# Kernel optimization log

Hardware: AMD Instinct MI355X
Metric: run time of the kernel (lower is better)

The kernel has to match this reference:

```python
import jax, jax.numpy as jnp
import numpy as np

N = 50000
E = 800000
D = 128
LN_EPS = 1e-5


def setup_inputs() -> dict:
    key = jax.random.key(0)
    k1, k2, k3, k4 = jax.random.split(key, 4)
    x = jax.random.normal(k1, (N, D), dtype=jnp.float32)
    edge_index = jax.random.randint(k2, (2, E), 0, N, dtype=jnp.int32)
    # xavier_uniform with gain=sqrt(2) (relu gain)
    gain = float(np.sqrt(2.0))
    lim_lin = gain * float(np.sqrt(6.0 / (D + D)))
    W_lin = jax.random.uniform(k3, (D, D), dtype=jnp.float32, minval=-lim_lin, maxval=lim_lin)
    lim_attn = gain * float(np.sqrt(6.0 / (2 * D + 1)))
    W_attn = jax.random.uniform(k4, (1, 2 * D), dtype=jnp.float32, minval=-lim_attn, maxval=lim_attn)
    ln_scale = jnp.ones((D,), dtype=jnp.float32)
    ln_bias = jnp.zeros((D,), dtype=jnp.float32)
    return {"x": x, "W_lin": W_lin, "W_attn": W_attn,
            "ln_scale": ln_scale, "ln_bias": ln_bias, "edge_index": edge_index}


def _layer_norm(h, scale, bias):
    mu = jnp.mean(h, axis=-1, keepdims=True)
    var = jnp.mean(jnp.square(h - mu), axis=-1, keepdims=True)
    return (h - mu) * jax.lax.rsqrt(var + LN_EPS) * scale + bias


def reference(x, W_lin, W_attn, ln_scale, ln_bias, edge_index):
    n = x.shape[0]
    src, dst = edge_index[0], edge_index[1]
    # h = x @ W_lin^T  [N, D]
    h = jnp.einsum('nd,od->no', x, W_lin)
    # attention score: [h_src || h_dst] @ W_attn^T == h_src@a_src + h_dst@a_dst
    d = h.shape[1]
    a_src = W_attn[0, :d]
    a_dst = W_attn[0, d:]
    s_src = h @ a_src  # [N]
    s_dst = h @ a_dst  # [N]
    scores = s_src[src] + s_dst[dst]  # [E]
    scores = jnp.where(scores >= 0, scores, 0.2 * scores)  # leaky_relu(0.2)
    # segment softmax over edges grouped by dst
    seg_max = jax.ops.segment_max(scores, dst, num_segments=n)  # [N]
    seg_max = jnp.where(jnp.isfinite(seg_max), seg_max, 0.0)
    ex = jnp.exp(scores - seg_max[dst])  # [E]
    denom = jax.ops.segment_sum(ex, dst, num_segments=n)  # [N]
    alpha = ex / jnp.where(denom > 0, denom, 1.0)[dst]  # [E]
    # weighted message aggregation (dropout is identity in eval mode)
    msgs = h[src] * alpha[:, None]  # [E, D]
    agg = jax.ops.segment_sum(msgs, dst, num_segments=n)  # [N, D]
    # residual (input_dim == output_dim -> no projection) + layer norm
    return _layer_norm(agg + x, ln_scale, ln_bias)
```

## Files before the change

### kernel.cpp

```cpp
#include <hip/hip_runtime.h>

#define N_NODES 50000
#define E_EDGES 800000
#define D_DIM   128
#define LN_EPS  1e-5f
#define SCAN_BLOCKS 196
#define GEMM_BLOCKS 391
#define HIST4_BLOCKS 782
#define SCAT_BLOCKS  782

typedef __bf16 bf16x8 __attribute__((ext_vector_type(8)));
typedef unsigned short ushort8v __attribute__((ext_vector_type(8)));
typedef float f32x4 __attribute__((ext_vector_type(4)));
typedef int i32x2v __attribute__((ext_vector_type(2)));
typedef int i32x16v __attribute__((ext_vector_type(16)));

__device__ inline unsigned short f2b(float f) {
    unsigned int u = __float_as_uint(f);
    unsigned int r = u + 0x7FFFu + ((u >> 16) & 1u);
    return (unsigned short)(r >> 16);
}
__device__ inline float b2f(unsigned short h) {
    return __uint_as_float((unsigned int)h << 16);
}
__device__ inline float blo(unsigned int u) { return __uint_as_float(u << 16); }
__device__ inline float bhi(unsigned int u) { return __uint_as_float(u & 0xFFFF0000u); }

__device__ inline i32x16v sload16(const uint2* p) {
    i32x16v r;
    asm volatile("s_load_dwordx16 %0, %1, 0x0\n\ts_waitcnt lgkmcnt(0)"
                 : "=&s"(r) : "s"(p));
    return r;
}
__device__ inline i32x2v sload2(const uint2* p) {
    i32x2v r;
    asm volatile("s_load_dwordx2 %0, %1, 0x0\n\ts_waitcnt lgkmcnt(0)"
                 : "=&s"(r) : "s"(p));
    return r;
}

__global__ void k_prep(const float* __restrict__ W,
                       unsigned short* __restrict__ Whp,
                       unsigned short* __restrict__ Wlp,
                       int* __restrict__ count) {
    int i = blockIdx.x * 256 + threadIdx.x;
    if (i < N_NODES) count[i] = 0;
    if (i < 16384) {
        int o = i >> 7, k = i & 127;
        float v = W[i];
        unsigned short h = f2b(v);
        unsigned short l = f2b(v - b2f(h));
        int idx = (k >> 3) * 1024 + o * 8 + (k & 7);
        Whp[idx] = h;
        Wlp[idx] = l;
    }
}

__global__ __launch_bounds__(256, 2) void k_gemm_hist(
        const float* __restrict__ x, const unsigned short* __restrict__ Wpk,
        const float* __restrict__ Wa, const int* __restrict__ dst,
        int* __restrict__ count, int* __restrict__ erank,
        unsigned short* __restrict__ hb,
        float* __restrict__ ssrc, float* __restrict__ sdst) {
    __shared__ float4 wl4[4096];
    const int tid = threadIdx.x;

    if (blockIdx.x >= GEMM_BLOCKS) {
        int e0 = (blockIdx.x - GEMM_BLOCKS) * 1024 + tid * 4;
        if (e0 < E_EDGES) {
            int4 dv = *(const int4*)&dst[e0];
            int r0 = atomicAdd(&count[dv.x], 1);
            int r1 = atomicAdd(&count[dv.y], 1);
            int r2 = atomicAdd(&count[dv.z], 1);
            int r3 = atomicAdd(&count[dv.w], 1);
            *(int4*)&erank[e0] = make_int4(r0, r1, r2, r3);
        }
        return;
    }

    {
        const float4* wsrc = (const float4*)Wpk;
        #pragma unroll
        for (int i = 0; i < 16; ++i)
            wl4[i * 256 + tid] = wsrc[i * 256 + tid];
    }

    const int c = tid & 15;
    const int g = (tid >> 4) & 3;
    const int w = tid >> 6;
    const int n0 = blockIdx.x * 128;

    bf16x8 ah[2][4], al[2][4];
    #pragma unroll
    for (int t = 0; t < 2; ++t) {
        int n = n0 + w * 32 + t * 16 + c;
        if (n > N_NODES - 1) n = N_NODES - 1;
        const float* xr = x + (size_t)n * 128;
        #pragma unroll
        for (int s = 0; s < 4; ++s) {
            float4 f0 = *(const float4*)(xr + s * 32 + g * 8);
            float4 f1 = *(const float4*)(xr + s * 32 + g * 8 + 4);
            float fv[8] = {f0.x, f0.y, f0.z, f0.w, f1.x, f1.y, f1.z, f1.w};
            ushort8v uh, ul;
            #pragma unroll
            for (int j = 0; j < 8; ++j) {
                unsigned short hj = f2b(fv[j]);
                uh[j] = hj;
                ul[j] = f2b(fv[j] - b2f(hj));
            }
            ah[t][s] = __builtin_bit_cast(bf16x8, uh);
            al[t][s] = __builtin_bit_cast(bf16x8, ul);
        }
    }

    __syncthreads();
    const bf16x8* wb = (const bf16x8*)wl4;

    f32x4 acc[2][8];
    #pragma unroll
    for (int t = 0; t < 2; ++t)
        #pragma unroll
        for (int cb = 0; cb < 8; ++cb)
            acc[t][cb] = (f32x4){0.f, 0.f, 0.f, 0.f};

    #pragma unroll
    for (int cb = 0; cb < 8; ++cb) {
        #pragma unroll
        for (int s = 0; s < 4; ++s) {
            int q = (s * 4 + g) * 128 + cb * 16 + c;
            bf16x8 bh = wb[q];
            bf16x8 bl = wb[2048 + q];
            acc[0][cb] = __builtin_amdgcn_mfma_f32_16x16x32_bf16(ah[0][s], bh, acc[0][cb], 0, 0, 0);
            acc[1][cb] = __builtin_amdgcn_mfma_f32_16x16x32_bf16(ah[1][s], bh, acc[1][cb], 0, 0, 0);
            acc[0][cb] = __builtin_amdgcn_mfma_f32_16x16x32_bf16(al[0][s], bh, acc[0][cb], 0, 0, 0);
            acc[1][cb] = __builtin_amdgcn_mfma_f32_16x16x32_bf16(al[1][s], bh, acc[1][cb], 0, 0, 0);
            acc[0][cb] = __builtin_amdgcn_mfma_f32_16x16x32_bf16(ah[0][s], bl, acc[0][cb], 0, 0, 0);
            acc[1][cb] = __builtin_amdgcn_mfma_f32_16x16x32_bf16(ah[1][s], bl, acc[1][cb], 0, 0, 0);
        }
    }

    float asv[8], adv[8];
    #pragma unroll
    for (int cb = 0; cb < 8; ++cb) {
        asv[cb] = Wa[cb * 16 + c];
        adv[cb] = Wa[128 + cb * 16 + c];
    }
    #pragma unroll
    for (int t = 0; t < 2; ++t) {
        #pragma unroll
        for (int i = 0; i < 4; ++i) {
            int n = n0 + w * 32 + t * 16 + g * 4 + i;
            float ps = 0.f, pd = 0.f;
            #pragma unroll
            for (int cb = 0; cb < 8; ++cb) {
                float v = acc[t][cb][i];
                ps += v * asv[cb];
                pd += v * adv[cb];
            }
            #pragma unroll
            for (int off = 1; off < 16; off <<= 1) {
                ps += __shfl_xor(ps, off);
                pd += __shfl_xor(pd, off);
            }
            if (c == 0 && n < N_NODES) { ssrc[n] = ps; sdst[n] = pd; }
        }
    }

    __syncthreads();
    unsigned short* hlds = (unsigned short*)wl4;
    #pragma unroll
    for (int t = 0; t < 2; ++t)
        #pragma unroll
        for (int cb = 0; cb < 8; ++cb)
            #pragma unroll
            for (int i = 0; i < 4; ++i)
                hlds[(w * 32 + t * 16 + g * 4 + i) * 128 + cb * 16 + c] =
                    f2b(acc[t][cb][i]);
    __syncthreads();
    #pragma unroll
    for (int ii = 0; ii < 8; ++ii) {
        int cidx = ii * 256 + tid;
        int row = cidx >> 4, off = cidx & 15;
        int n = n0 + row;
        if (n < N_NODES) {
            ushort8v v = *(const ushort8v*)&hlds[row * 128 + off * 8];
            *(ushort8v*)&hb[(size_t)n * 128 + off * 8] = v;
        }
    }
}

__global__ __launch_bounds__(256) void k_scan1(const int* __restrict__ count,
                                               int* __restrict__ rowptr,
                                               int* __restrict__ bsum) {
    __shared__ int wsum[4];
    const int tid  = threadIdx.x;
    const int lane = tid & 63, w = tid >> 6;
    int i = blockIdx.x * 256 + tid;
    int v = (i < N_NODES) ? count[i] : 0;
    int sc = v;
    #pragma unroll
    for (int off = 1; off < 64; off <<= 1) {
        int t = __shfl_up(sc, off);
        if (lane >= off) sc += t;
    }
    if (lane == 63) wsum[w] = sc;
    __syncthreads();
    if (tid == 0) {
        int s0 = wsum[0], s1 = wsum[1], s2 = wsum[2], s3 = wsum[3];
        wsum[0] = 0; wsum[1] = s0; wsum[2] = s0 + s1; wsum[3] = s0 + s1 + s2;
        bsum[blockIdx.x] = s0 + s1 + s2 + s3;
    }
    __syncthreads();
    if (i < N_NODES) rowptr[i] = sc - v + wsum[w];
}

__global__ __launch_bounds__(256) void k_scan2(int* __restrict__ bsum) {
    __shared__ int wsum[4];
    const int tid  = threadIdx.x;
    const int lane = tid & 63, w = tid >> 6;
    int v = (tid < SCAN_BLOCKS) ? bsum[tid] : 0;
    int sc = v;
    #pragma unroll
    for (int off = 1; off < 64; off <<= 1) {
        int t = __shfl_up(sc, off);
        if (lane >= off) sc += t;
    }
    if (lane == 63) wsum[w] = sc;
    __syncthreads();
    if (tid == 0) {
        int s0 = wsum[0], s1 = wsum[1], s2 = wsum[2];
        wsum[3] = s0 + s1 + s2; wsum[2] = s0 + s1; wsum[1] = s0; wsum[0] = 0;
    }
    __syncthreads();
    if (tid < SCAN_BLOCKS) bsum[tid] = sc - v + wsum[w];
}

__global__ __launch_bounds__(256) void k_scatter(
        const int* __restrict__ src, const int* __restrict__ dst,
        const int* __restrict__ erank,
        const float* __restrict__ ssrc, const float* __restrict__ sdst,
        const int* __restrict__ rowptr, const int* __restrict__ bsum,
        uint2* __restrict__ sev) {
    int e0 = (blockIdx.x * 256 + threadIdx.x) * 4;
    if (e0 >= E_EDGES) return;
    int4 sv = *(const int4*)&src[e0];
    int4 dv = *(const int4*)&dst[e0];
    int4 rk = *(const int4*)&erank[e0];
    float ss0 = ssrc[sv.x], ss1 = ssrc[sv.y], ss2 = ssrc[sv.z], ss3 = ssrc[sv.w];
    float sd0 = sdst[dv.x], sd1 = sdst[dv.y], sd2 = sdst[dv.z], sd3 = sdst[dv.w];
    int rp0 = rowptr[dv.x], rp1 = rowptr[dv.y], rp2 = rowptr[dv.z], rp3 = rowptr[dv.w];
    int bs0 = bsum[dv.x >> 8], bs1 = bsum[dv.y >> 8];
    int bs2 = bsum[dv.z >> 8], bs3 = bsum[dv.w >> 8];
    float c0 = ss0 + sd0, c1 = ss1 + sd1, c2 = ss2 + sd2, c3 = ss3 + sd3;
    c0 = c0 >= 0.f ? c0 : 0.2f * c0;
    c1 = c1 >= 0.f ? c1 : 0.2f * c1;
    c2 = c2 >= 0.f ? c2 : 0.2f * c2;
    c3 = c3 >= 0.f ? c3 : 0.2f * c3;
    sev[rp0 + bs0 + rk.x] = make_uint2((unsigned int)sv.x, __float_as_uint(__expf(c0)));
    sev[rp1 + bs1 + rk.y] = make_uint2((unsigned int)sv.y, __float_as_uint(__expf(c1)));
    sev[rp2 + bs2 + rk.z] = make_uint2((unsigned int)sv.z, __float_as_uint(__expf(c2)));
    sev[rp3 + bs3 + rk.w] = make_uint2((unsigned int)sv.w, __float_as_uint(__expf(c3)));
}

__global__ __launch_bounds__(256) void k_gather(
        const int* __restrict__ rowptr, const int* __restrict__ bsum,
        const uint2* __restrict__ sev,
        const unsigned short* __restrict__ hb, const float* __restrict__ x,
        const float* __restrict__ scale, const float* __restrict__ bias,
        float* __restrict__ out) {
    int n    = __builtin_amdgcn_readfirstlane(blockIdx.x * 4 + (threadIdx.x >> 6));
    int lane = threadIdx.x & 63;
    int beg = rowptr[n] + bsum[n >> 8];
    int end = (n == N_NODES - 1) ? E_EDGES : rowptr[n + 1] + bsum[(n + 1) >> 8];
    const unsigned int* hb32 = (const unsigned int*)hb;

    float a0 = 0.f, a1 = 0.f, b0 = 0.f, b1 = 0.f, den = 0.f, den2 = 0.f;

    int i = beg;
    for (; i + 15 < end; i += 16) {
        int ib = __builtin_amdgcn_readfirstlane(i);
        i32x16v s0 = sload16(sev + ib);
        i32x16v s1 = sload16(sev + ib + 8);
        unsigned int u[16];
        #pragma unroll
        for (int q = 0; q < 8; ++q)
            u[q] = hb32[(((unsigned)s0[2 * q]) << 6) + lane];
        #pragma unroll
        for (int q = 0; q < 8; ++q)
            u[8 + q] = hb32[(((unsigned)s1[2 * q]) << 6) + lane];
        #pragma unroll
        for (int q = 0; q < 8; q += 2) {
            float ex0 = __uint_as_float(s0[2 * q + 1]);
            float ex1 = __uint_as_float(s0[2 * q + 3]);
            den  += ex0; den2 += ex1;
            a0 += ex0 * blo(u[q]);     a1 += ex0 * bhi(u[q]);
            b0 += ex1 * blo(u[q + 1]); b1 += ex1 * bhi(u[q + 1]);
        }
        #pragma unroll
        for (int q = 0; q < 8; q += 2) {
            float ex0 = __uint_as_float(s1[2 * q + 1]);
            float ex1 = __uint_as_float(s1[2 * q + 3]);
            den  += ex0; den2 += ex1;
            a0 += ex0 * blo(u[8 + q]);     a1 += ex0 * bhi(u[8 + q]);
            b0 += ex1 * blo(u[8 + q + 1]); b1 += ex1 * bhi(u[8 + q + 1]);
        }
    }
    for (; i + 7 < end; i += 8) {
        int ib = __builtin_amdgcn_readfirstlane(i);
        i32x16v s0 = sload16(sev + ib);
        unsigned int u[8];
        #pragma unroll
        for (int q = 0; q < 8; ++q)
            u[q] = hb32[(((unsigned)s0[2 * q]) << 6) + lane];
        #pragma unroll
        for (int q = 0; q < 8; q += 2) {
            float ex0 = __uint_as_float(s0[2 * q + 1]);
            float ex1 = __uint_as_float(s0[2 * q + 3]);
            den  += ex0; den2 += ex1;
            a0 += ex0 * blo(u[q]);     a1 += ex0 * bhi(u[q]);
            b0 += ex1 * blo(u[q + 1]); b1 += ex1 * bhi(u[q + 1]);
        }
    }
    for (; i < end; ++i) {
        i32x2v p2 = sload2(sev + __builtin_amdgcn_readfirstlane(i));
        unsigned int u0 = hb32[(((unsigned)p2[0]) << 6) + lane];
        float ex0 = __uint_as_float(p2[1]);
        den += ex0;
        a0 += ex0 * blo(u0);
        a1 += ex0 * bhi(u0);
    }
    a0 += b0; a1 += b1; den += den2;

    float inv_d = 1.f / (den > 0.f ? den : 1.f);
    size_t base = (size_t)n * 128 + 2 * lane;
    float2 xv = *(const float2*)&x[base];
    float r0 = a0 * inv_d + xv.x;
    float r1 = a1 * inv_d + xv.y;

    float sum = r0 + r1;
    #pragma unroll
    for (int off = 32; off >= 1; off >>= 1) sum += __shfl_xor(sum, off);
    float mu = sum * (1.f / 128.f);
    float d0 = r0 - mu, d1 = r1 - mu;
    float ss = d0 * d0 + d1 * d1;
    #pragma unroll
    for (int off = 32; off >= 1; off >>= 1) ss += __shfl_xor(ss, off);
    float inv = rsqrtf(ss * (1.f / 128.f) + LN_EPS);
    float o0 = d0 * inv * scale[2 * lane]     + bias[2 * lane];
    float o1 = d1 * inv * scale[2 * lane + 1] + bias[2 * lane + 1];
    *(float2*)&out[base] = make_float2(o0, o1);
}

extern "C" void kernel_launch(void* const* d_in, const int* in_sizes, int n_in,
                              void* d_out, int out_size, void* d_ws, size_t ws_size,
                              hipStream_t stream) {
    const float* x        = (const float*)d_in[0];
    const float* W_lin    = (const float*)d_in[1];
    const float* W_attn   = (const float*)d_in[2];
    const float* ln_scale = (const float*)d_in[3];
    const float* ln_bias  = (const float*)d_in[4];
    const int*   edge     = (const int*)d_in[5];
    const int*   e_src    = edge;
    const int*   e_dst    = edge + E_EDGES;
    float* out = (float*)d_out;

    char* ws = (char*)d_ws;
    unsigned short* hb  = (unsigned short*)(ws);
    unsigned short* Whp = (unsigned short*)(ws + 12800000);
    unsigned short* Wlp = (unsigned short*)(ws + 12832768);
    float* ssrc   = (float*)(ws + 12865536);
    float* sdst   = (float*)(ws + 13065536);
    int*   count  = (int*)  (ws + 13265536);
    int*   rowptr = (int*)  (ws + 13465536);
    int*   bsum   = (int*)  (ws + 13665552);
    uint2* sev    = (uint2*)(ws + 13666352);
    int*   erank  = (int*)  (ws + 20066352);

    k_prep     <<<SCAN_BLOCKS, 256, 0, stream>>>(W_lin, Whp, Wlp, count);
    k_gemm_hist<<<GEMM_BLOCKS + HIST4_BLOCKS, 256, 0, stream>>>(
                    x, Whp, W_attn, e_dst, count, erank, hb, ssrc, sdst);
    k_scan1    <<<SCAN_BLOCKS, 256, 0, stream>>>(count, rowptr, bsum);
    k_scan2    <<<1,    256, 0, stream>>>(bsum);
    k_scatter  <<<SCAT_BLOCKS, 256, 0, stream>>>(e_src, e_dst, erank, ssrc, sdst,
                                                 rowptr, bsum, sev);
    k_gather   <<<12500, 256, 0, stream>>>(rowptr, bsum, sev, hb, x,
                                           ln_scale, ln_bias, out);
}
```

Before: 179.5 us.

## Split gather into column-sliced partial aggregation plus separate layernorm pass

Replaces the single per-node gather kernel with a column-sliced gather: each node's 128 features are split into four 32-column slices handled by separate waves, with two edges processed per wave using half-waves. Partial aggregates and denominators are written to global memory, and a new final kernel applies normalization, the residual and layernorm. The two scan kernels are merged using a last-block-done atomic, and scatter now handles 8 edges per thread. The aim is more parallelism and lower latency in the gather, at the cost of an extra full-size intermediate buffer round trip, 2-byte scattered loads instead of 4-byte ones, and an extra kernel launch.

Measured after the change: 258.5 us. +44.0%, slower.

```diff
diff --git a/kernel.cpp b/kernel.cpp
--- a/kernel.cpp
+++ b/kernel.cpp
@@ -7,7 +7,9 @@
 #define SCAN_BLOCKS 196
 #define GEMM_BLOCKS 391
 #define HIST4_BLOCKS 782
-#define SCAT_BLOCKS  782
+#define SCAT_BLOCKS  391
+#define GSLICE_BLOCKS 50000
+#define FINAL_BLOCKS 12500
 
 typedef __bf16 bf16x8 __attribute__((ext_vector_type(8)));
 typedef unsigned short ushort8v __attribute__((ext_vector_type(8)));
@@ -23,8 +25,6 @@
 __device__ inline float b2f(unsigned short h) {
     return __uint_as_float((unsigned int)h << 16);
 }
-__device__ inline float blo(unsigned int u) { return __uint_as_float(u << 16); }
-__device__ inline float bhi(unsigned int u) { return __uint_as_float(u & 0xFFFF0000u); }
 
 __device__ inline i32x16v sload16(const uint2* p) {
     i32x16v r;
@@ -42,8 +42,9 @@
 __global__ void k_prep(const float* __restrict__ W,
                        unsigned short* __restrict__ Whp,
                        unsigned short* __restrict__ Wlp,
-                       int* __restrict__ count) {
+                       int* __restrict__ count, int* __restrict__ done) {
     int i = blockIdx.x * 256 + threadIdx.x;
+    if (i == 0) *done = 0;
     if (i < N_NODES) count[i] = 0;
     if (i < 16384) {
         int o = i >> 7, k = i & 127;
@@ -57,7 +58,7 @@
 }
 
 __global__ __launch_bounds__(256, 2) void k_gemm_hist(
-        const float* __restrict__ x, const unsigned short* __restrict__ Wpk,
+        const float* __restrict__ xin, const unsigned short* __restrict__ Wpk,
         const float* __restrict__ Wa, const int* __restrict__ dst,
         int* __restrict__ count, int* __restrict__ erank,
         unsigned short* __restrict__ hb,
@@ -95,7 +96,7 @@
     for (int t = 0; t < 2; ++t) {
         int n = n0 + w * 32 + t * 16 + c;
         if (n > N_NODES - 1) n = N_NODES - 1;
-        const float* xr = x + (size_t)n * 128;
+        const float* xr = xin + (size_t)n * 128;
         #pragma unroll
         for (int s = 0; s < 4; ++s) {
             float4 f0 = *(const float4*)(xr + s * 32 + g * 8);
@@ -189,10 +190,12 @@
     }
 }
 
-__global__ __launch_bounds__(256) void k_scan1(const int* __restrict__ count,
-                                               int* __restrict__ rowptr,
-                                               int* __restrict__ bsum) {
+__global__ __launch_bounds__(256) void k_scan(const int* __restrict__ count,
+                                              int* __restrict__ rowptr,
+                                              int* __restrict__ bsum,
+                                              int* __restrict__ done) {
     __shared__ int wsum[4];
+    __shared__ int amLast;
     const int tid  = threadIdx.x;
     const int lane = tid & 63, w = tid >> 6;
     int i = blockIdx.x * 256 + tid;
@@ -212,27 +215,28 @@
     }
     __syncthreads();
     if (i < N_NODES) rowptr[i] = sc - v + wsum[w];
-}
-
-__global__ __launch_bounds__(256) void k_scan2(int* __restrict__ bsum) {
-    __shared__ int wsum[4];
-    const int tid  = threadIdx.x;
-    const int lane = tid & 63, w = tid >> 6;
-    int v = (tid < SCAN_BLOCKS) ? bsum[tid] : 0;
-    int sc = v;
+
+    __threadfence();
+    if (tid == 0) amLast = (atomicAdd(done, 1) == SCAN_BLOCKS - 1);
+    __syncthreads();
+    if (!amLast) return;
+    __threadfence();
+    int v2 = (tid < SCAN_BLOCKS) ? bsum[tid] : 0;
+    int sc2 = v2;
     #pragma unroll
     for (int off = 1; off < 64; off <<= 1) {
-        int t = __shfl_up(sc, off);
-        if (lane >= off) sc += t;
-    }
-    if (lane == 63) wsum[w] = sc;
+        int t = __shfl_up(sc2, off);
+        if (lane >= off) sc2 += t;
+    }
+    __syncthreads();
+    if (lane == 63) wsum[w] = sc2;
     __syncthreads();
     if (tid == 0) {
         int s0 = wsum[0], s1 = wsum[1], s2 = wsum[2];
         wsum[3] = s0 + s1 + s2; wsum[2] = s0 + s1; wsum[1] = s0; wsum[0] = 0;
     }
     __syncthreads();
-    if (tid < SCAN_BLOCKS) bsum[tid] = sc - v + wsum[w];
+    if (tid < SCAN_BLOCKS) bsum[tid] = sc2 - v2 + wsum[w];
 }
 
 __global__ __launch_bounds__(256) void k_scatter(
@@ -241,101 +245,90 @@
         const float* __restrict__ ssrc, const float* __restrict__ sdst,
         const int* __restrict__ rowptr, const int* __restrict__ bsum,
         uint2* __restrict__ sev) {
-    int e0 = (blockIdx.x * 256 + threadIdx.x) * 4;
+    int e0 = (blockIdx.x * 256 + threadIdx.x) * 8;
     if (e0 >= E_EDGES) return;
-    int4 sv = *(const int4*)&src[e0];
-    int4 dv = *(const int4*)&dst[e0];
-    int4 rk = *(const int4*)&erank[e0];
-    float ss0 = ssrc[sv.x], ss1 = ssrc[sv.y], ss2 = ssrc[sv.z], ss3 = ssrc[sv.w];
-    float sd0 = sdst[dv.x], sd1 = sdst[dv.y], sd2 = sdst[dv.z], sd3 = sdst[dv.w];
-    int rp0 = rowptr[dv.x], rp1 = rowptr[dv.y], rp2 = rowptr[dv.z], rp3 = rowptr[dv.w];
-    int bs0 = bsum[dv.x >> 8], bs1 = bsum[dv.y >> 8];
-    int bs2 = bsum[dv.z >> 8], bs3 = bsum[dv.w >> 8];
-    float c0 = ss0 + sd0, c1 = ss1 + sd1, c2 = ss2 + sd2, c3 = ss3 + sd3;
-    c0 = c0 >= 0.f ? c0 : 0.2f * c0;
-    c1 = c1 >= 0.f ? c1 : 0.2f * c1;
-    c2 = c2 >= 0.f ? c2 : 0.2f * c2;
-    c3 = c3 >= 0.f ? c3 : 0.2f * c3;
-    sev[rp0 + bs0 + rk.x] = make_uint2((unsigned int)sv.x, __float_as_uint(__expf(c0)));
-    sev[rp1 + bs1 + rk.y] = make_uint2((unsigned int)sv.y, __float_as_uint(__expf(c1)));
-    sev[rp2 + bs2 + rk.z] = make_uint2((unsigned int)sv.z, __float_as_uint(__expf(c2)));
-    sev[rp3 + bs3 + rk.w] = make_uint2((unsigned int)sv.w, __float_as_uint(__expf(c3)));
-}
-
-__global__ __launch_bounds__(256) void k_gather(
+    int sv[8], dv[8], rk[8];
+    *(int4*)&sv[0] = *(const int4*)&src[e0];
+    *(int4*)&sv[4] = *(const int4*)&src[e0 + 4];
+    *(int4*)&dv[0] = *(const int4*)&dst[e0];
+    *(int4*)&dv[4] = *(const int4*)&dst[e0 + 4];
+    *(int4*)&rk[0] = *(const int4*)&erank[e0];
+    *(int4*)&rk[4] = *(const int4*)&erank[e0 + 4];
+    float ssv[8], sdv[8];
+    int rp[8], bs[8];
+    #pragma unroll
+    for (int q = 0; q < 8; ++q) {
+        ssv[q] = ssrc[sv[q]];
+        sdv[q] = sdst[dv[q]];
+        rp[q]  = rowptr[dv[q]];
+        bs[q]  = bsum[dv[q] >> 8];
+    }
+    #pragma unroll
+    for (int q = 0; q < 8; ++q) {
+        float sc = ssv[q] + sdv[q];
+        sc = sc >= 0.f ? sc : 0.2f * sc;
+        sev[rp[q] + bs[q] + rk[q]] =
+            make_uint2((unsigned int)sv[q], __float_as_uint(__expf(sc)));
+    }
+}
+
+__global__ __launch_bounds__(256) void k_gslice(
         const int* __restrict__ rowptr, const int* __restrict__ bsum,
-        const uint2* __restrict__ sev,
-        const unsigned short* __restrict__ hb, const float* __restrict__ x,
+        const uint2* __restrict__ sev, const unsigned short* __restrict__ hb,
+        float* __restrict__ part, float* __restrict__ den) {
+    const int bid   = blockIdx.x;
+    const int xb    = bid & 7;
+    const int slice = xb >> 1;
+    const int grp   = (bid >> 3) * 2 + (xb & 1);
+    const int n     = __builtin_amdgcn_readfirstlane(grp * 4 + (threadIdx.x >> 6));
+    const int lane  = threadIdx.x & 63;
+    const int el    = lane >> 5, sl = lane & 31;
+    int beg = rowptr[n] + bsum[n >> 8];
+    int end = (n == N_NODES - 1) ? E_EDGES : rowptr[n + 1] + bsum[(n + 1) >> 8];
+    const unsigned short* hs = hb + slice * 32 + sl;
+
+    float a = 0.f, dn = 0.f;
+    int i = beg;
+    for (; i + 7 < end; i += 8) {
+        i32x16v s0 = sload16(sev + __builtin_amdgcn_readfirstlane(i));
+        #pragma unroll
+        for (int q = 0; q < 4; ++q) {
+            int srcA = s0[4 * q], srcB = s0[4 * q + 2];
+            float exA = __uint_as_float(s0[4 * q + 1]);
+            float exB = __uint_as_float(s0[4 * q + 3]);
+            int srcq = el ? srcB : srcA;
+            unsigned short u = hs[(size_t)srcq * 128];
+            float ex = el ? exB : exA;
+            a  += ex * b2f(u);
+            dn += exA + exB;
+        }
+    }
+    for (; i < end; ++i) {
+        i32x2v p2 = sload2(sev + __builtin_amdgcn_readfirstlane(i));
+        unsigned short u = hs[(size_t)p2[0] * 128];
+        float ex = __uint_as_float(p2[1]);
+        a  += (el ? 0.f : ex * b2f(u));
+        dn += ex;
+    }
+    a += __shfl_xor(a, 32);
+    if (lane < 32) part[(size_t)n * 128 + slice * 32 + sl] = a;
+    if (slice == 0 && lane == 0) den[n] = dn;
+}
+
+__global__ __launch_bounds__(256) void k_final(
+        const float* __restrict__ part, const float* __restrict__ den,
+        const float* __restrict__ xin,
         const float* __restrict__ scale, const float* __restrict__ bias,
         float* __restrict__ out) {
-    int n    = __builtin_amdgcn_readfirstlane(blockIdx.x * 4 + (threadIdx.x >> 6));
+    int n    = blockIdx.x * 4 + (threadIdx.x >> 6);
     int lane = threadIdx.x & 63;
-    int beg = rowptr[n] + bsum[n >> 8];
-    int end = (n == N_NODES - 1) ? E_EDGES : rowptr[n + 1] + bsum[(n + 1) >> 8];
-    const unsigned int* hb32 = (const unsigned int*)hb;
-
-    float a0 = 0.f, a1 = 0.f, b0 = 0.f, b1 = 0.f, den = 0.f, den2 = 0.f;
-
-    int i = beg;
-    for (; i + 15 < end; i += 16) {
-        int ib = __builtin_amdgcn_readfirstlane(i);
-        i32x16v s0 = sload16(sev + ib);
-        i32x16v s1 = sload16(sev + ib + 8);
-        unsigned int u[16];
-        #pragma unroll
-        for (int q = 0; q < 8; ++q)
-            u[q] = hb32[(((unsigned)s0[2 * q]) << 6) + lane];
-        #pragma unroll
-        for (int q = 0; q < 8; ++q)
-            u[8 + q] = hb32[(((unsigned)s1[2 * q]) << 6) + lane];
-        #pragma unroll
-        for (int q = 0; q < 8; q += 2) {
-            float ex0 = __uint_as_float(s0[2 * q + 1]);
-            float ex1 = __uint_as_float(s0[2 * q + 3]);
-            den  += ex0; den2 += ex1;
-            a0 += ex0 * blo(u[q]);     a1 += ex0 * bhi(u[q]);
-            b0 += ex1 * blo(u[q + 1]); b1 += ex1 * bhi(u[q + 1]);
-        }
-        #pragma unroll
-        for (int q = 0; q < 8; q += 2) {
-            float ex0 = __uint_as_float(s1[2 * q + 1]);
-            float ex1 = __uint_as_float(s1[2 * q + 3]);
-            den  += ex0; den2 += ex1;
-            a0 += ex0 * blo(u[8 + q]);     a1 += ex0 * bhi(u[8 + q]);
-            b0 += ex1 * blo(u[8 + q + 1]); b1 += ex1 * bhi(u[8 + q + 1]);
-        }
-    }
-    for (; i + 7 < end; i += 8) {
-        int ib = __builtin_amdgcn_readfirstlane(i);
-        i32x16v s0 = sload16(sev + ib);
-        unsigned int u[8];
-        #pragma unroll
-        for (int q = 0; q < 8; ++q)
-            u[q] = hb32[(((unsigned)s0[2 * q]) << 6) + lane];
-        #pragma unroll
-        for (int q = 0; q < 8; q += 2) {
-            float ex0 = __uint_as_float(s0[2 * q + 1]);
-            float ex1 = __uint_as_float(s0[2 * q + 3]);
-            den  += ex0; den2 += ex1;
-            a0 += ex0 * blo(u[q]);     a1 += ex0 * bhi(u[q]);
-            b0 += ex1 * blo(u[q + 1]); b1 += ex1 * bhi(u[q + 1]);
-        }
-    }
-    for (; i < end; ++i) {
-        i32x2v p2 = sload2(sev + __builtin_amdgcn_readfirstlane(i));
-        unsigned int u0 = hb32[(((unsigned)p2[0]) << 6) + lane];
-        float ex0 = __uint_as_float(p2[1]);
-        den += ex0;
-        a0 += ex0 * blo(u0);
-        a1 += ex0 * bhi(u0);
-    }
-    a0 += b0; a1 += b1; den += den2;
-
-    float inv_d = 1.f / (den > 0.f ? den : 1.f);
+    float dn = den[n];
+    float inv_d = 1.f / (dn > 0.f ? dn : 1.f);
     size_t base = (size_t)n * 128 + 2 * lane;
-    float2 xv = *(const float2*)&x[base];
-    float r0 = a0 * inv_d + xv.x;
-    float r1 = a1 * inv_d + xv.y;
+    float2 pv = *(const float2*)&part[base];
+    float2 xv = *(const float2*)&xin[base];
+    float r0 = pv.x * inv_d + xv.x;
+    float r1 = pv.y * inv_d + xv.y;
 
     float sum = r0 + r1;
     #pragma unroll
@@ -375,14 +368,17 @@
     int*   bsum   = (int*)  (ws + 13665552);
     uint2* sev    = (uint2*)(ws + 13666352);
     int*   erank  = (int*)  (ws + 20066352);
-
-    k_prep     <<<SCAN_BLOCKS, 256, 0, stream>>>(W_lin, Whp, Wlp, count);
+    float* part   = (float*)(ws + 23266432);
+    float* den    = (float*)(ws + 48866432);
+    int*   done   = (int*)  (ws + 49066432);
+
+    k_prep     <<<SCAN_BLOCKS, 256, 0, stream>>>(W_lin, Whp, Wlp, count, done);
     k_gemm_hist<<<GEMM_BLOCKS + HIST4_BLOCKS, 256, 0, stream>>>(
                     x, Whp, W_attn, e_dst, count, erank, hb, ssrc, sdst);
-    k_scan1    <<<SCAN_BLOCKS, 256, 0, stream>>>(count, rowptr, bsum);
-    k_scan2    <<<1,    256, 0, stream>>>(bsum);
+    k_scan     <<<SCAN_BLOCKS, 256, 0, stream>>>(count, rowptr, bsum, done);
     k_scatter  <<<SCAT_BLOCKS, 256, 0, stream>>>(e_src, e_dst, erank, ssrc, sdst,
                                                  rowptr, bsum, sev);
-    k_gather   <<<12500, 256, 0, stream>>>(rowptr, bsum, sev, hb, x,
-                                           ln_scale, ln_bias, out);
-}
+    k_gslice   <<<GSLICE_BLOCKS, 256, 0, stream>>>(rowptr, bsum, sev, hb, part, den);
+    k_final    <<<FINAL_BLOCKS, 256, 0, stream>>>(part, den, x,
+                                                  ln_scale, ln_bias, out);
+}
```

## Fuse scan passes via last-block pattern, halve scatter work per thread, overlap scalar loads

Applied to the files above, without the earlier changes.

The two-kernel prefix scan becomes one kernel: the last block to finish, detected through an atomic counter that k_prep resets, scans the block sums. This removes one kernel launch and its dependency gap. k_scatter now handles 2 edges per thread instead of 4, with twice as many blocks, to raise parallelism for the random gathers. In the gather kernel, the two scalar loads of each 16-edge chunk are issued back to back before a single wait, so their latencies overlap.

After: 189.9 us. 5.8% more time.

```diff
diff --git a/kernel.cpp b/kernel.cpp
--- a/kernel.cpp
+++ b/kernel.cpp
@@ -7,7 +7,8 @@
 #define SCAN_BLOCKS 196
 #define GEMM_BLOCKS 391
 #define HIST4_BLOCKS 782
-#define SCAT_BLOCKS  782
+#define SCAT_BLOCKS 1563
+#define GATH_BLOCKS 12500
 
 typedef __bf16 bf16x8 __attribute__((ext_vector_type(8)));
 typedef unsigned short ushort8v __attribute__((ext_vector_type(8)));
@@ -26,11 +27,14 @@
 __device__ inline float blo(unsigned int u) { return __uint_as_float(u << 16); }
 __device__ inline float bhi(unsigned int u) { return __uint_as_float(u & 0xFFFF0000u); }
 
-__device__ inline i32x16v sload16(const uint2* p) {
+__device__ inline i32x16v sload16_nw(const uint2* p) {
     i32x16v r;
-    asm volatile("s_load_dwordx16 %0, %1, 0x0\n\ts_waitcnt lgkmcnt(0)"
-                 : "=&s"(r) : "s"(p));
+    asm volatile("s_load_dwordx16 %0, %1, 0x0" : "=&s"(r) : "s"(p));
     return r;
+}
+__device__ inline void swait() {
+    asm volatile("s_waitcnt lgkmcnt(0)");
+    __builtin_amdgcn_sched_barrier(0);
 }
 __device__ inline i32x2v sload2(const uint2* p) {
     i32x2v r;
@@ -42,8 +46,9 @@
 __global__ void k_prep(const float* __restrict__ W,
                        unsigned short* __restrict__ Whp,
                        unsigned short* __restrict__ Wlp,
-                       int* __restrict__ count) {
+                       int* __restrict__ count, int* __restrict__ done) {
     int i = blockIdx.x * 256 + threadIdx.x;
+    if (i == 0) *done = 0;
     if (i < N_NODES) count[i] = 0;
     if (i < 16384) {
         int o = i >> 7, k = i & 127;
@@ -57,7 +62,7 @@
 }
 
 __global__ __launch_bounds__(256, 2) void k_gemm_hist(
-        const float* __restrict__ x, const unsigned short* __restrict__ Wpk,
+        const float* __restrict__ xin, const unsigned short* __restrict__ Wpk,
         const float* __restrict__ Wa, const int* __restrict__ dst,
         int* __restrict__ count, int* __restrict__ erank,
         unsigned short* __restrict__ hb,
@@ -95,7 +100,7 @@
     for (int t = 0; t < 2; ++t) {
         int n = n0 + w * 32 + t * 16 + c;
         if (n > N_NODES - 1) n = N_NODES - 1;
-        const float* xr = x + (size_t)n * 128;
+        const float* xr = xin + (size_t)n * 128;
         #pragma unroll
         for (int s = 0; s < 4; ++s) {
             float4 f0 = *(const float4*)(xr + s * 32 + g * 8);
@@ -189,10 +194,12 @@
     }
 }
 
-__global__ __launch_bounds__(256) void k_scan1(const int* __restrict__ count,
-                                               int* __restrict__ rowptr,
-                                               int* __restrict__ bsum) {
+__global__ __launch_bounds__(256) void k_scan(const int* __restrict__ count,
+                                              int* __restrict__ rowptr,
+                                              int* __restrict__ bsum,
+                                              int* __restrict__ done) {
     __shared__ int wsum[4];
+    __shared__ int amLast;
     const int tid  = threadIdx.x;
     const int lane = tid & 63, w = tid >> 6;
     int i = blockIdx.x * 256 + tid;
@@ -212,27 +219,28 @@
     }
     __syncthreads();
     if (i < N_NODES) rowptr[i] = sc - v + wsum[w];
-}
-
-__global__ __launch_bounds__(256) void k_scan2(int* __restrict__ bsum) {
-    __shared__ int wsum[4];
-    const int tid  = threadIdx.x;
-    const int lane = tid & 63, w = tid >> 6;
-    int v = (tid < SCAN_BLOCKS) ? bsum[tid] : 0;
-    int sc = v;
+
+    __threadfence();
+    if (tid == 0) amLast = (atomicAdd(done, 1) == SCAN_BLOCKS - 1);
+    __syncthreads();
+    if (!amLast) return;
+    __threadfence();
+    int v2 = (tid < SCAN_BLOCKS) ? bsum[tid] : 0;
+    int sc2 = v2;
     #pragma unroll
     for (int off = 1; off < 64; off <<= 1) {
-        int t = __shfl_up(sc, off);
-        if (lane >= off) sc += t;
-    }
-    if (lane == 63) wsum[w] = sc;
+        int t = __shfl_up(sc2, off);
+        if (lane >= off) sc2 += t;
+    }
+    __syncthreads();
+    if (lane == 63) wsum[w] = sc2;
     __syncthreads();
     if (tid == 0) {
         int s0 = wsum[0], s1 = wsum[1], s2 = wsum[2];
         wsum[3] = s0 + s1 + s2; wsum[2] = s0 + s1; wsum[1] = s0; wsum[0] = 0;
     }
     __syncthreads();
-    if (tid < SCAN_BLOCKS) bsum[tid] = sc - v + wsum[w];
+    if (tid < SCAN_BLOCKS) bsum[tid] = sc2 - v2 + wsum[w];
 }
 
 __global__ __launch_bounds__(256) void k_scatter(
@@ -241,25 +249,20 @@
         const float* __restrict__ ssrc, const float* __restrict__ sdst,
         const int* __restrict__ rowptr, const int* __restrict__ bsum,
         uint2* __restrict__ sev) {
-    int e0 = (blockIdx.x * 256 + threadIdx.x) * 4;
+    int e0 = (blockIdx.x * 256 + threadIdx.x) * 2;
     if (e0 >= E_EDGES) return;
-    int4 sv = *(const int4*)&src[e0];
-    int4 dv = *(const int4*)&dst[e0];
-    int4 rk = *(const int4*)&erank[e0];
-    float ss0 = ssrc[sv.x], ss1 = ssrc[sv.y], ss2 = ssrc[sv.z], ss3 = ssrc[sv.w];
-    float sd0 = sdst[dv.x], sd1 = sdst[dv.y], sd2 = sdst[dv.z], sd3 = sdst[dv.w];
-    int rp0 = rowptr[dv.x], rp1 = rowptr[dv.y], rp2 = rowptr[dv.z], rp3 = rowptr[dv.w];
+    int2 sv = *(const int2*)&src[e0];
+    int2 dv = *(const int2*)&dst[e0];
+    int2 rk = *(const int2*)&erank[e0];
+    float ss0 = ssrc[sv.x], ss1 = ssrc[sv.y];
+    float sd0 = sdst[dv.x], sd1 = sdst[dv.y];
+    int rp0 = rowptr[dv.x], rp1 = rowptr[dv.y];
     int bs0 = bsum[dv.x >> 8], bs1 = bsum[dv.y >> 8];
-    int bs2 = bsum[dv.z >> 8], bs3 = bsum[dv.w >> 8];
-    float c0 = ss0 + sd0, c1 = ss1 + sd1, c2 = ss2 + sd2, c3 = ss3 + sd3;
+    float c0 = ss0 + sd0, c1 = ss1 + sd1;
     c0 = c0 >= 0.f ? c0 : 0.2f * c0;
     c1 = c1 >= 0.f ? c1 : 0.2f * c1;
-    c2 = c2 >= 0.f ? c2 : 0.2f * c2;
-    c3 = c3 >= 0.f ? c3 : 0.2f * c3;
     sev[rp0 + bs0 + rk.x] = make_uint2((unsigned int)sv.x, __float_as_uint(__expf(c0)));
     sev[rp1 + bs1 + rk.y] = make_uint2((unsigned int)sv.y, __float_as_uint(__expf(c1)));
-    sev[rp2 + bs2 + rk.z] = make_uint2((unsigned int)sv.z, __float_as_uint(__expf(c2)));
-    sev[rp3 + bs3 + rk.w] = make_uint2((unsigned int)sv.w, __float_as_uint(__expf(c3)));
 }
 
 __global__ __launch_bounds__(256) void k_gather(
@@ -279,8 +282,9 @@
     int i = beg;
     for (; i + 15 < end; i += 16) {
         int ib = __builtin_amdgcn_readfirstlane(i);
-        i32x16v s0 = sload16(sev + ib);
-        i32x16v s1 = sload16(sev + ib + 8);
+        i32x16v s0 = sload16_nw(sev + ib);
+        i32x16v s1 = sload16_nw(sev + ib + 8);
+        swait();
         unsigned int u[16];
         #pragma unroll
         for (int q = 0; q < 8; ++q)
@@ -307,7 +311,8 @@
     }
     for (; i + 7 < end; i += 8) {
         int ib = __builtin_amdgcn_readfirstlane(i);
-        i32x16v s0 = sload16(sev + ib);
+        i32x16v s0 = sload16_nw(sev + ib);
+        swait();
         unsigned int u[8];
         #pragma unroll
         for (int q = 0; q < 8; ++q)
@@ -375,14 +380,14 @@
     int*   bsum   = (int*)  (ws + 13665552);
     uint2* sev    = (uint2*)(ws + 13666352);
     int*   erank  = (int*)  (ws + 20066352);
-
-    k_prep     <<<SCAN_BLOCKS, 256, 0, stream>>>(W_lin, Whp, Wlp, count);
+    int*   done   = (int*)  (ws + 23266352);
+
+    k_prep     <<<SCAN_BLOCKS, 256, 0, stream>>>(W_lin, Whp, Wlp, count, done);
     k_gemm_hist<<<GEMM_BLOCKS + HIST4_BLOCKS, 256, 0, stream>>>(
                     x, Whp, W_attn, e_dst, count, erank, hb, ssrc, sdst);
-    k_scan1    <<<SCAN_BLOCKS, 256, 0, stream>>>(count, rowptr, bsum);
-    k_scan2    <<<1,    256, 0, stream>>>(bsum);
+    k_scan     <<<SCAN_BLOCKS, 256, 0, stream>>>(count, rowptr, bsum, done);
     k_scatter  <<<SCAT_BLOCKS, 256, 0, stream>>>(e_src, e_dst, erank, ssrc, sdst,
                                                  rowptr, bsum, sev);
-    k_gather   <<<12500, 256, 0, stream>>>(rowptr, bsum, sev, hb, x,
-                                           ln_scale, ln_bias, out);
-}
+    k_gather   <<<GATH_BLOCKS, 256, 0, stream>>>(rowptr, bsum, sev, hb, x,
+                                                 ln_scale, ln_bias, out);
+}
```
